# Performance work log

Hardware: AMD Instinct MI355X
Metric: run time of the kernel (lower is better)

## Reference

```python
import jax, jax.numpy as jnp
import numpy as np

N = 50000   # nodes
E = 300000  # directed edges
IN = 512
H = 256
OUT = 256
K = 4096    # K_target; since K < N, pooled node count Kc == K statically


def setup_inputs() -> dict:
    key = jax.random.key(0)
    ks = jax.random.split(key, 8)
    x = jax.random.normal(ks[0], (N, IN), jnp.float32)
    edge_index = jax.random.randint(ks[1], (2, E), 0, N)
    W1 = jax.random.normal(ks[2], (IN, H), jnp.float32) / np.float32(np.sqrt(IN))
    b1 = jnp.zeros((H,), jnp.float32)
    W2 = jax.random.normal(ks[3], (H, OUT), jnp.float32) / np.float32(np.sqrt(H))
    b2 = jnp.zeros((OUT,), jnp.float32)
    w_score = jax.random.normal(ks[4], (H,), jnp.float32) / np.float32(np.sqrt(H))
    W_skip = jax.random.normal(ks[5], (H, OUT), jnp.float32) / np.float32(np.sqrt(H))
    b_skip = jnp.zeros((OUT,), jnp.float32)
    return dict(x=x, edge_index=edge_index, W1=W1, b1=b1, W2=W2, b2=b2,
                w_score=w_score, W_skip=W_skip, b_skip=b_skip)


def _gcn_sparse(x, src, dst, W, b, n):
    # PyG GCNConv(add_self_loops=True, normalize=True): out = D^{-1/2}(A+I)D^{-1/2} x W + b,
    # degrees computed on dst after adding self loops.
    h = x @ W
    loop = jnp.arange(n)
    s = jnp.concatenate([src, loop])
    d = jnp.concatenate([dst, loop])
    deg = jax.ops.segment_sum(jnp.ones_like(d, h.dtype), d, num_segments=n)
    dinv = jnp.where(deg > 0, jax.lax.rsqrt(deg), 0.0)
    coef = (dinv[s] * dinv[d])[:, None]
    return jax.ops.segment_sum(h[s] * coef, d, num_segments=n) + b


def _forward(x, edge_index, W1, b1, W2, b2, w_score, W_skip, b_skip):
    n = x.shape[0]
    src, dst = edge_index[0], edge_index[1]

    # conv1 + relu (dropout is identity in eval mode)
    x1 = jax.nn.relu(_gcn_sparse(x, src, dst, W1, b1, n))
    raw = x1 @ w_score                       # [N] score (Linear, no bias)
    x1g = x1 * jnp.tanh(raw)[:, None]        # gated features

    # top-K node selection
    _, kept = jax.lax.top_k(raw, K)          # sorted descending, like torch.topk
    keep_mask = jnp.zeros((n,), bool).at[kept].set(True)
    deg = jax.ops.segment_sum(jnp.ones((src.shape[0],), jnp.int32), src, num_segments=n)

    # cluster ids: kept nodes get 0..K-1 in topk order
    cid = jnp.full((n,), -1, jnp.int32).at[kept].set(jnp.arange(K, dtype=jnp.int32))

    # non-kept nodes join the kept (undirected) neighbor with max degree;
    # encode (degree, -node_id) so segment_max picks max degree, tie-break smallest id
    s_all = jnp.concatenate([src, dst])
    t_all = jnp.concatenate([dst, src])
    cand = jnp.where(keep_mask[t_all], deg[t_all] * n + (n - 1 - t_all), -1)
    best = jax.ops.segment_max(cand, s_all, num_segments=n)  # empty segs -> int min
    has = best >= 0
    best_t = (n - 1) - jnp.where(has, best % n, 0)
    # global fallback: kept node with max degree (tie-break: earliest in topk order)
    enc_k = deg[kept] * K + (K - 1 - jnp.arange(K))
    bg = kept[jnp.argmax(enc_k)]
    cid = jnp.where(keep_mask, cid, jnp.where(has, cid[best_t], cid[bg]))

    # mean pooling per cluster (pool_by_partition)
    sums = jax.ops.segment_sum(x1g, cid, num_segments=K)
    cnt = jnp.maximum(jax.ops.segment_sum(jnp.ones((n,), x.dtype), cid, num_segments=K), 1.0)
    xp = sums / cnt[:, None]

    # pooled edges with dedup + self-pair removal, as dense KxK adjacency (rows = dst)
    cu, cv = cid[src], cid[dst]
    A = jnp.zeros((K, K), x.dtype).at[cv, cu].max((cu != cv).astype(x.dtype))
    Ahat = A + jnp.eye(K, dtype=x.dtype)
    di = jax.lax.rsqrt(Ahat.sum(axis=1))     # deg >= 1 from self loops
    An = di[:, None] * Ahat * di[None, :]

    # conv2 on pooled graph, broadcast back, skip connection
    xp2 = An @ (xp @ W2) + b2
    return xp2[cid] + x1 @ W_skip + b_skip


def reference(x, edge_index, W1, b1, W2, b2, w_score, W_skip, b_skip):
    return _forward(x, edge_index, W1, b1, W2, b2, w_score, W_skip, b_skip)
```

## Files before the change

### kernel.cpp

```cpp
#include <hip/hip_runtime.h>
#include <hip/hip_bf16.h>

#define N_NODES 50000
#define E_EDGES 300000
#define IN_F 512
#define H_F 256
#define OUT_F 256
#define K_CL 4096
#define KW (K_CL / 32)
#define PCH 128
#define THRESH 192
#define MAXH 1024
#define NSPL 32
#define NB2 ((N_NODES + 255) / 256)

typedef short bh8 __attribute__((ext_vector_type(8)));
typedef float f4 __attribute__((ext_vector_type(4)));
typedef unsigned short u16;

__device__ __forceinline__ unsigned fkey(float f) {
    unsigned u = __float_as_uint(f);
    return (u & 0x80000000u) ? ~u : (u | 0x80000000u);
}

__device__ __forceinline__ u16 f2bf(float f) {
    __hip_bfloat16 b = __float2bfloat16(f);
    return *reinterpret_cast<u16*>(&b);
}

__global__ __launch_bounds__(256) void init_nodes(int* cntD, int* degS,
                                                  unsigned long long* best_enc,
                                                  int* bgnode, int* heavycnt,
                                                  unsigned long long* bestpack) {
    int i = blockIdx.x * blockDim.x + threadIdx.x;
    if (i < N_NODES) { cntD[i] = 0; degS[i] = 0; best_enc[i] = 0ULL; }
    if (i == 0) { *heavycnt = 0; *bgnode = 0x7FFFFFFF; *bestpack = 0ULL; }
}

__global__ __launch_bounds__(256) void deg_edges(const int* __restrict__ src,
                                                 const int* __restrict__ dst,
                                                 int* cntD, int* degS) {
    int e = blockIdx.x * blockDim.x + threadIdx.x;
    if (e >= E_EDGES) return;
    atomicAdd(&cntD[dst[e]], 1);
    atomicAdd(&degS[src[e]], 1);
}

__global__ __launch_bounds__(256) void make_dinv(const int* __restrict__ cntD, float* dinv) {
    int i = blockIdx.x * blockDim.x + threadIdx.x;
    if (i < N_NODES) dinv[i] = rsqrtf((float)cntD[i] + 1.0f);
}

#define SBM 64
#define SBN 128
#define SBK 16
#define SAPAD 4
__global__ __launch_bounds__(256) void gemm_f32s(const float* __restrict__ A,
                                                 const float* __restrict__ B,
                                                 float* __restrict__ C,
                                                 int M, int Nc, int Kd) {
    __shared__ float As[2][SBK][SBM + SAPAD];
    __shared__ float Bs[2][SBK][SBN];
    int tid = threadIdx.x;
    int tx = tid & 15;
    int ty = tid >> 4;
    int lane = tid & 63;
    int wave = tid >> 6;
    int row0 = blockIdx.y * SBM, col0 = blockIdx.x * SBN;
    float acc[4][8] = {};

    int ar = tid >> 2;
    int akq = tid & 3;

    auto stage_B = [&](int k0, int bb) {
        #pragma unroll
        for (int u = 0; u < 2; ++u) {
            int chunk = wave * 2 + u;
            int krow = chunk * 2 + (lane >> 5);
            const float* gsrc = &B[(long)(k0 + krow) * Nc + col0 + (lane & 31) * 4];
            __builtin_amdgcn_global_load_lds(
                (const __attribute__((address_space(1))) void*)gsrc,
                (__attribute__((address_space(3))) void*)&Bs[bb][chunk * 2][0],
                16, 0, 0);
        }
    };
    auto stage_A = [&](int k0, int bb) {
        int gr = row0 + ar;
        float4 v = {0.f, 0.f, 0.f, 0.f};
        if (gr < M) v = *(const float4*)&A[(long)gr * Kd + k0 + akq * 4];
        As[bb][akq * 4 + 0][ar] = v.x;
        As[bb][akq * 4 + 1][ar] = v.y;
        As[bb][akq * 4 + 2][ar] = v.z;
        As[bb][akq * 4 + 3][ar] = v.w;
    };
    auto compute = [&](int bb) {
        #pragma unroll
        for (int k = 0; k < SBK; ++k) {
            float4 a0 = *(const float4*)&As[bb][k][ty * 4];
            float4 b0 = *(const float4*)&Bs[bb][k][tx * 4];
            float4 b1 = *(const float4*)&Bs[bb][k][tx * 4 + 64];
            float av[4] = {a0.x, a0.y, a0.z, a0.w};
            float bv[8] = {b0.x, b0.y, b0.z, b0.w, b1.x, b1.y, b1.z, b1.w};
            #pragma unroll
            for (int i = 0; i < 4; ++i)
                #pragma unroll
                for (int j = 0; j < 8; ++j)
                    acc[i][j] += av[i] * bv[j];
        }
    };

    stage_B(0, 0);
    stage_A(0, 0);
    __syncthreads();
    int nt = Kd / SBK;
    for (int t = 0; t < nt; ++t) {
        int cb = t & 1;
        if (t + 1 < nt) {
            stage_B(SBK * (t + 1), cb ^ 1);
            stage_A(SBK * (t + 1), cb ^ 1);
        }
        compute(cb);
        __syncthreads();
    }

    #pragma unroll
    for (int i = 0; i < 4; ++i) {
        int gr = row0 + ty * 4 + i;
        if (gr >= M) continue;
        float4 o0 = {acc[i][0], acc[i][1], acc[i][2], acc[i][3]};
        float4 o1 = {acc[i][4], acc[i][5], acc[i][6], acc[i][7]};
        *(float4*)&C[(long)gr * Nc + col0 + tx * 4] = o0;
        *(float4*)&C[(long)gr * Nc + col0 + 64 + tx * 4] = o1;
    }
}

__global__ __launch_bounds__(256) void conv_bf16(const float* __restrict__ src,
                                                 u16* __restrict__ dst,
                                                 const int* __restrict__ cnt, long total4) {
    long i = (long)blockIdx.x * 256 + threadIdx.x;
    if (i >= total4) return;
    float s = 1.f;
    if (cnt) { int row = (int)(i >> 6); s = 1.f / fmaxf((float)cnt[row], 1.f); }
    float4 v = ((const float4*)src)[i];
    ushort4 o;
    o.x = f2bf(v.x * s); o.y = f2bf(v.y * s);
    o.z = f2bf(v.z * s); o.w = f2bf(v.w * s);
    ((ushort4*)dst)[i] = o;
}

__global__ __launch_bounds__(256) void pack_W(const float* __restrict__ W, u16* __restrict__ Bp) {
    int k = blockIdx.x;
    int col = threadIdx.x;
    int kb = k >> 5, g = (k >> 3) & 3, j = k & 7;
    Bp[(((long)(kb * 4 + g) * 256) + col) * 8 + j] = f2bf(W[(long)k * 256 + col]);
}

__global__ __launch_bounds__(256) void gemm_mfma(const u16* __restrict__ Ab,
                                                 const u16* __restrict__ Bp,
                                                 float* __restrict__ C,
                                                 int M,
                                                 const int* __restrict__ cid,
                                                 const float* __restrict__ xp2,
                                                 const float* __restrict__ bskip) {
    int tid = threadIdx.x;
    int w = tid >> 6, l = tid & 63;
    int lo16 = l & 15, hi4 = l >> 4;
    int arow = blockIdx.x * 64 + w * 16 + lo16;
    f4 acc[16];
    #pragma unroll
    for (int n = 0; n < 16; ++n) acc[n] = (f4){0.f, 0.f, 0.f, 0.f};

    #pragma unroll
    for (int kb = 0; kb < 8; ++kb) {
        bh8 a = {0, 0, 0, 0, 0, 0, 0, 0};
        if (arow < M) a = *(const bh8*)&Ab[(long)arow * 256 + kb * 32 + hi4 * 8];
        const u16* bbase = &Bp[(((long)(kb * 4 + hi4)) * 256 + lo16) * 8];
        #pragma unroll
        for (int n = 0; n < 16; ++n) {
            bh8 b = *(const bh8*)&bbase[(long)n * 128];
            acc[n] = __builtin_amdgcn_mfma_f32_16x16x32_bf16(a, b, acc[n], 0, 0, 0);
        }
    }

    int orow0 = blockIdx.x * 64 + w * 16 + hi4 * 4;
    #pragma unroll
    for (int r = 0; r < 4; ++r) {
        int gr = orow0 + r;
        if (gr >= M) continue;
        long rb = (long)gr * 256;
        const float* xrow = cid ? (xp2 + (long)cid[gr] * 256) : nullptr;
        #pragma unroll
        for (int n = 0; n < 16; ++n) {
            int gc = n * 16 + lo16;
            float v = acc[n][r];
            if (cid) v += xrow[gc] + bskip[gc];
            C[rb + gc] = v;
        }
    }
}

__global__ __launch_bounds__(256) void scan_l1(const int* __restrict__ cnt,
                                               int* bsum, int n) {
    __shared__ int s[256];
    int t = threadIdx.x;
    int i = blockIdx.x * 256 + t;
    s[t] = (i < n) ? cnt[i] : 0;
    __syncthreads();
    for (int off = 128; off > 0; off >>= 1) {
        if (t < off) s[t] += s[t + off];
        __syncthreads();
    }
    if (t == 0) bsum[blockIdx.x] = s[0];
}

__global__ __launch_bounds__(256) void scan_l2(const int* __restrict__ bsum,
                                               int* bstart, int nb) {
    __shared__ int s[256];
    int t = threadIdx.x;
    int v = (t < nb) ? bsum[t] : 0;
    s[t] = v;
    __syncthreads();
    for (int off = 1; off < 256; off <<= 1) {
        int a = (t >= off) ? s[t - off] : 0;
        __syncthreads();
        s[t] += a;
        __syncthreads();
    }
    if (t < nb) bstart[t] = s[t] - v;
}

__global__ __launch_bounds__(256) void scan_l3(const int* __restrict__ cnt,
                                               const int* __restrict__ bstart,
                                               int* start, int* cur, int n) {
    __shared__ int s[256];
    int t = threadIdx.x;
    int i = blockIdx.x * 256 + t;
    int v = (i < n) ? cnt[i] : 0;
    s[t] = v;
    __syncthreads();
    for (int off = 1; off < 256; off <<= 1) {
        int a = (t >= off) ? s[t - off] : 0;
        __syncthreads();
        s[t] += a;
        __syncthreads();
    }
    int st = bstart[blockIdx.x] + s[t] - v;
    if (i < n) { start[i] = st; cur[i] = st; }
    if (i == n - 1) start[n] = st + v;
}

__global__ __launch_bounds__(256) void csr_scatter(const int* __restrict__ src,
                                                   const int* __restrict__ dst,
                                                   int* cur, int* csr) {
    int e = blockIdx.x * blockDim.x + threadIdx.x;
    if (e >= E_EDGES) return;
    int d = dst[e];
    int p = atomicAdd(&cur[d], 1);
    csr[p] = src[e];
}

__global__ __launch_bounds__(256) void agg_fused(const float* __restrict__ h,
                                                 const float* __restrict__ dinv,
                                                 const int* __restrict__ rowptr,
                                                 const int* __restrict__ csr,
                                                 const float* __restrict__ b1,
                                                 const float* __restrict__ w_score,
                                                 float* x1, u16* x1b, float* raw) {
    __shared__ int s_src[128];
    __shared__ float s_cf[128];
    __shared__ float red[256];
    int i = blockIdx.x, j = threadIdx.x;
    float di_ = dinv[i];
    float acc = di_ * di_ * h[(long)i * H_F + j];
    int p0 = rowptr[i], p1 = rowptr[i + 1];
    for (int base = p0; base < p1; base += 128) {
        int m = p1 - base; if (m > 128) m = 128;
        if (j < m) { int s = csr[base + j]; s_src[j] = s; s_cf[j] = dinv[s]; }
        __syncthreads();
        #pragma unroll 4
        for (int t = 0; t < m; ++t)
            acc += (s_cf[t] * di_) * h[(long)s_src[t] * H_F + j];
        __syncthreads();
    }
    float v = fmaxf(acc + b1[j], 0.f);
    x1[(long)i * H_F + j] = v;
    x1b[(long)i * H_F + j] = f2bf(v);
    red[j] = v * w_score[j];
    __syncthreads();
    for (int off = 128; off > 0; off >>= 1) {
        if (j < off) red[j] += red[j + off];
        __syncthreads();
    }
    if (j == 0) raw[i] = red[0];
}

__global__ __launch_bounds__(1024) void topk_select(const float* __restrict__ raw,
                                                    unsigned* outT, int* outNeedEq) {
    __shared__ unsigned hist[256];
    __shared__ unsigned sh_prefix;
    __shared__ int sh_k;
    int tid = threadIdx.x;
    if (tid == 0) { sh_prefix = 0; sh_k = K_CL; }
    __syncthreads();
    for (int byte = 3; byte >= 0; --byte) {
        if (tid < 256) hist[tid] = 0;
        __syncthreads();
        unsigned prefix = sh_prefix;
        unsigned known_mask = (byte == 3) ? 0u : (0xFFFFFFFFu << ((byte + 1) * 8));
        for (int i = tid; i < N_NODES; i += 1024) {
            unsigned key = fkey(raw[i]);
            if ((key & known_mask) == prefix)
                atomicAdd(&hist[(key >> (byte * 8)) & 255], 1u);
        }
        __syncthreads();
        if (tid == 0) {
            int kk = sh_k;
            int cum = 0;
            int v = 255;
            for (; v > 0; --v) {
                int c = (int)hist[v];
                if (cum + c >= kk) break;
                cum += c;
            }
            sh_prefix = prefix | ((unsigned)v << (byte * 8));
            sh_k = kk - cum;
        }
        __syncthreads();
    }
    if (tid == 0) { *outT = sh_prefix; *outNeedEq = sh_k; }
}

__global__ __launch_bounds__(256) void topk_count(const float* __restrict__ raw,
                                                  const unsigned* pT,
                                                  int* bGt, int* bEq) {
    __shared__ int sg[256], se[256];
    unsigned T = *pT;
    int t = threadIdx.x;
    int i = blockIdx.x * 256 + t;
    int gt = 0, eq = 0;
    if (i < N_NODES) {
        unsigned k = fkey(raw[i]);
        gt = k > T; eq = (k == T);
    }
    sg[t] = gt; se[t] = eq;
    __syncthreads();
    for (int off = 128; off > 0; off >>= 1) {
        if (t < off) { sg[t] += sg[t + off]; se[t] += se[t + off]; }
        __syncthreads();
    }
    if (t == 0) { bGt[blockIdx.x] = sg[0]; bEq[blockIdx.x] = se[0]; }
}

__global__ __launch_bounds__(256) void scan_blocks(const int* __restrict__ bGt,
                                                   const int* __restrict__ bEq,
                                                   int* gtStart, int* eqStart) {
    __shared__ int sg[256], se[256];
    int t = threadIdx.x;
    int vg = (t < NB2) ? bGt[t] : 0;
    int ve = (t < NB2) ? bEq[t] : 0;
    sg[t] = vg; se[t] = ve;
    __syncthreads();
    for (int off = 1; off < 256; off <<= 1) {
        int a = (t >= off) ? sg[t - off] : 0;
        int b = (t >= off) ? se[t - off] : 0;
        __syncthreads();
        sg[t] += a; se[t] += b;
        __syncthreads();
    }
    if (t < NB2) { gtStart[t] = sg[t] - vg; eqStart[t] = se[t] - ve; }
    if (t == 255) gtStart[NB2] = sg[255];
}

__global__ __launch_bounds__(256) void topk_assign(const float* __restrict__ raw,
                                                   const unsigned* pT, const int* pNeedEq,
                                                   const int* __restrict__ degS,
                                                   const int* __restrict__ gtStart,
                                                   const int* __restrict__ eqStart,
                                                   int* keep, int* cid,
                                                   unsigned long long* bestpack) {
    __shared__ int sg[256], se[256];
    unsigned T = *pT;
    int needEq = *pNeedEq;
    int totalGt = gtStart[NB2];
    int b = blockIdx.x, t = threadIdx.x;
    int i = b * 256 + t;
    int gt = 0, eq = 0;
    unsigned k = 0;
    if (i < N_NODES) {
        k = fkey(raw[i]);
        gt = k > T; eq = (k == T);
    }
    sg[t] = gt; se[t] = eq;
    __syncthreads();
    for (int off = 1; off < 256; off <<= 1) {
        int a = (t >= off) ? sg[t - off] : 0;
        int c = (t >= off) ? se[t - off] : 0;
        __syncthreads();
        sg[t] += a; se[t] += c;
        __syncthreads();
    }
    int eg = sg[t] - gt, ee = se[t] - eq;
    int kp = 0;
    unsigned long long p = 0ULL;
    if (i < N_NODES) {
        int c = -1;
        if (gt) { kp = 1; c = gtStart[b] + eg; }
        else if (eq) {
            int r = eqStart[b] + ee;
            if (r < needEq) { kp = 1; c = totalGt + r; }
        }
        keep[i] = kp; cid[i] = c;
        if (kp) p = ((unsigned long long)(unsigned)degS[i] << 32) | k;
    }
    #pragma unroll
    for (int o = 32; o > 0; o >>= 1) {
        unsigned long long q = __shfl_xor((long long)p, o, 64);
        if (q > p) p = q;
    }
    if ((t & 63) == 0 && p) atomicMax(bestpack, p);
}

__global__ __launch_bounds__(256) void bg_node(const int* __restrict__ keep,
                                               const int* __restrict__ degS,
                                               const float* __restrict__ raw,
                                               const unsigned long long* bestpack, int* bgnode) {
    int i = blockIdx.x * blockDim.x + threadIdx.x;
    if (i < N_NODES && keep[i]) {
        unsigned long long p = ((unsigned long long)(unsigned)degS[i] << 32) | fkey(raw[i]);
        if (p == *bestpack) atomicMin(bgnode, i);
    }
}

__global__ __launch_bounds__(256) void neigh_edges(const int* __restrict__ src,
                                                   const int* __restrict__ dst,
                                                   const int* __restrict__ keep,
                                                   const int* __restrict__ degS,
                                                   unsigned long long* best_enc) {
    int e = blockIdx.x * blockDim.x + threadIdx.x;
    if (e >= 2 * E_EDGES) return;
    int s, t;
    if (e < E_EDGES) { s = src[e]; t = dst[e]; }
    else { s = dst[e - E_EDGES]; t = src[e - E_EDGES]; }
    if (!keep[s] && keep[t]) {
        unsigned long long enc =
            (unsigned long long)((long long)degS[t] * N_NODES + (N_NODES - 1 - t)) + 1ULL;
        atomicMax(&best_enc[s], enc);
    }
}

__global__ __launch_bounds__(256) void resolve_cid(const int* __restrict__ keep,
                                                   const unsigned long long* __restrict__ best_enc,
                                                   const int* __restrict__ bgnode, int* cid) {
    int i = blockIdx.x * blockDim.x + threadIdx.x;
    if (i >= N_NODES) return;
    if (keep[i]) return;
    unsigned long long v = best_enc[i];
    if (v > 0ULL) {
        long long enc = (long long)(v - 1ULL);
        int t = (N_NODES - 1) - (int)(enc % N_NODES);
        cid[i] = cid[t];
    } else {
        cid[i] = cid[*bgnode];
    }
}

#define NPB 1024
__global__ __launch_bounds__(256) void ccount2(const int* __restrict__ cid, int* ccnt) {
    __shared__ int hist[K_CL];
    for (int t = threadIdx.x; t < K_CL; t += 256) hist[t] = 0;
    __syncthreads();
    int base = blockIdx.x * NPB;
    #pragma unroll
    for (int u = 0; u < NPB / 256; ++u) {
        int idx = base + u * 256 + threadIdx.x;
        if (idx < N_NODES) atomicAdd(&hist[cid[idx]], 1);
    }
    __syncthreads();
    for (int t = threadIdx.x; t < K_CL; t += 256) {
        int hh = hist[t];
        if (hh) atomicAdd(&ccnt[t], hh);
    }
}

__global__ __launch_bounds__(256) void cscatter2(const int* __restrict__ cid,
                                                 int* ccur, int* clist) {
    __shared__ int hist[K_CL];
    for (int t = threadIdx.x; t < K_CL; t += 256) hist[t] = 0;
    __syncthreads();
    int base = blockIdx.x * NPB;
    int myc[NPB / 256], myr[NPB / 256];
    #pragma unroll
    for (int u = 0; u < NPB / 256; ++u) {
        int idx = base + u * 256 + threadIdx.x;
        if (idx < N_NODES) { myc[u] = cid[idx]; myr[u] = atomicAdd(&hist[myc[u]], 1); }
        else myc[u] = -1;
    }
    __syncthreads();
    for (int t = threadIdx.x; t < K_CL; t += 256) {
        int hh = hist[t];
        if (hh) hist[t] = atomicAdd(&ccur[t], hh);
    }
    __syncthreads();
    #pragma unroll
    for (int u = 0; u < NPB / 256; ++u)
        if (myc[u] >= 0) clist[hist[myc[u]] + myr[u]] = base + u * 256 + threadIdx.x;
}

__global__ __launch_bounds__(256) void pool_chunk(const float* __restrict__ x1,
                                                  const float* __restrict__ raw,
                                                  const int* __restrict__ clist,
                                                  const int* __restrict__ cid,
                                                  float* xp) {
    __shared__ int s_node[PCH];
    __shared__ int s_c[PCH];
    __shared__ float s_g[PCH];
    int j = threadIdx.x;
    int base = blockIdx.x * PCH;
    int m = N_NODES - base; if (m > PCH) m = PCH;
    for (int t = j; t < m; t += 256) {
        int nd = clist[base + t];
        s_node[t] = nd;
        s_c[t] = cid[nd];
        s_g[t] = tanhf(raw[nd]);
    }
    __syncthreads();
    float acc = 0.f;
    int cprev = s_c[0];
    for (int t = 0; t < m; t += 4) {
        int mm = m - t; if (mm > 4) mm = 4;
        float v[4];
        #pragma unroll
        for (int u = 0; u < 4; ++u)
            if (u < mm) v[u] = x1[(long)s_node[t + u] * H_F + j];
        #pragma unroll
        for (int u = 0; u < 4; ++u) {
            if (u < mm) {
                int c = s_c[t + u];
                if (c != cprev) {
                    atomicAdd(&xp[(long)cprev * H_F + j], acc);
                    acc = 0.f;
                    cprev = c;
                }
                acc += s_g[t + u] * v[u];
            }
        }
    }
    atomicAdd(&xp[(long)cprev * H_F + j], acc);
}

__global__ __launch_bounds__(256) void build_Abits(const int* __restrict__ src,
                                                   const int* __restrict__ dst,
                                                   const int* __restrict__ cid,
                                                   unsigned* Abits) {
    int e = blockIdx.x * blockDim.x + threadIdx.x;
    if (e >= E_EDGES) return;
    int cu = cid[src[e]], cv = cid[dst[e]];
    if (cu != cv) atomicOr(&Abits[(long)cv * KW + (cu >> 5)], 1u << (cu & 31));
}

__global__ __launch_bounds__(256) void pop_di2(const unsigned* __restrict__ Abits, float* di,
                                               int* nnzA, int* heavy, int* heavycnt) {
    int i = blockIdx.x * blockDim.x + threadIdx.x;
    if (i >= K_CL) return;
    int c = 0;
    for (int w = 0; w < KW; ++w) c += __popc(Abits[(long)i * KW + w]);
    di[i] = rsqrtf((float)c + 1.0f);
    nnzA[i] = c;
    if (c > THRESH) {
        int p = atomicAdd(heavycnt, 1);
        if (p < MAXH) heavy[p] = i;
    }
}

__global__ __launch_bounds__(256) void spmm_light(const unsigned* __restrict__ Abits,
                                                  const float* __restrict__ xpW2,
                                                  const float* __restrict__ di,
                                                  const float* __restrict__ b2,
                                                  const int* __restrict__ nnzA,
                                                  float* xp2) {
    __shared__ unsigned s_row[KW];
    __shared__ float s_part[3][256];
    int cv = blockIdx.x;
    if (nnzA[cv] > THRESH) return;
    int tid = threadIdx.x;
    int w = tid >> 6, l = tid & 63;
    if (tid < KW) s_row[tid] = Abits[(long)cv * KW + tid];
    __syncthreads();
    float4 a0 = {0.f, 0.f, 0.f, 0.f}, a1 = {0.f, 0.f, 0.f, 0.f};
    const float4* Y4 = (const float4*)xpW2;
    for (int wi = w * 32; wi < w * 32 + 32; wi += 2) {
        unsigned w0 = s_row[wi], w1 = s_row[wi + 1];
        while (w0 | w1) {
            if (w0) {
                int b = __ffs(w0) - 1; w0 &= w0 - 1;
                int cu = wi * 32 + b;
                float d = di[cu];
                float4 y = Y4[(long)cu * 64 + l];
                a0.x += d * y.x; a0.y += d * y.y; a0.z += d * y.z; a0.w += d * y.w;
            }
            if (w1) {
                int b = __ffs(w1) - 1; w1 &= w1 - 1;
                int cu = (wi + 1) * 32 + b;
                float d = di[cu];
                float4 y = Y4[(long)cu * 64 + l];
                a1.x += d * y.x; a1.y += d * y.y; a1.z += d * y.z; a1.w += d * y.w;
            }
        }
    }
    float4 acc = {a0.x + a1.x, a0.y + a1.y, a0.z + a1.z, a0.w + a1.w};
    if (w > 0) *(float4*)&s_part[w - 1][l * 4] = acc;
    __syncthreads();
    if (w == 0) {
        #pragma unroll
        for (int ww = 0; ww < 3; ++ww) {
            float4 p = *(float4*)&s_part[ww][l * 4];
            acc.x += p.x; acc.y += p.y; acc.z += p.z; acc.w += p.w;
        }
        float dv = di[cv];
        float4 ys = Y4[(long)cv * 64 + l];
        float4 o;
        o.x = dv * (acc.x + dv * ys.x) + b2[l * 4 + 0];
        o.y = dv * (acc.y + dv * ys.y) + b2[l * 4 + 1];
        o.z = dv * (acc.z + dv * ys.z) + b2[l * 4 + 2];
        o.w = dv * (acc.w + dv * ys.w) + b2[l * 4 + 3];
        *(float4*)&xp2[(long)cv * H_F + l * 4] = o;
    }
}

__global__ __launch_bounds__(256) void spmm_heavy(const unsigned* __restrict__ Abits,
                                                  const float* __restrict__ xpW2,
                                                  const float* __restrict__ di,
                                                  const int* __restrict__ heavy,
                                                  const int* __restrict__ heavycnt,
                                                  float* Zacc) {
    __shared__ float s_part[3][256];
    int hi = blockIdx.x;
    int cnt = *heavycnt; if (cnt > MAXH) cnt = MAXH;
    if (hi >= cnt) return;
    int cv = heavy[hi];
    int sp = blockIdx.y;
    int tid = threadIdx.x;
    int w = tid >> 6, l = tid & 63;
    int wi = sp * (KW / NSPL) + w;
    unsigned word = Abits[(long)cv * KW + wi];
    float4 acc = {0.f, 0.f, 0.f, 0.f};
    const float4* Y4 = (const float4*)xpW2;
    while (word) {
        int b = __ffs(word) - 1; word &= word - 1;
        int cu = wi * 32 + b;
        float d = di[cu];
        float4 y = Y4[(long)cu * 64 + l];
        acc.x += d * y.x; acc.y += d * y.y; acc.z += d * y.z; acc.w += d * y.w;
    }
    if (w > 0) *(float4*)&s_part[w - 1][l * 4] = acc;
    __syncthreads();
    if (w == 0) {
        #pragma unroll
        for (int ww = 0; ww < 3; ++ww) {
            float4 p = *(float4*)&s_part[ww][l * 4];
            acc.x += p.x; acc.y += p.y; acc.z += p.z; acc.w += p.w;
        }
        float* zp = &Zacc[(long)cv * H_F + l * 4];
        atomicAdd(zp + 0, acc.x);
        atomicAdd(zp + 1, acc.y);
        atomicAdd(zp + 2, acc.z);
        atomicAdd(zp + 3, acc.w);
    }
}

__global__ __launch_bounds__(256) void heavy_epi(const float* __restrict__ Zacc,
                                                 const float* __restrict__ xpW2,
                                                 const float* __restrict__ di,
                                                 const float* __restrict__ b2,
                                                 const int* __restrict__ heavy,
                                                 const int* __restrict__ heavycnt,
                                                 float* xp2) {
    int hi = blockIdx.x;
    int cnt = *heavycnt; if (cnt > MAXH) cnt = MAXH;
    if (hi >= cnt) return;
    int cv = heavy[hi];
    int j = threadIdx.x;
    float dv = di[cv];
    xp2[(long)cv * H_F + j] =
        dv * (Zacc[(long)cv * H_F + j] + dv * xpW2[(long)cv * H_F + j]) + b2[j];
}

static inline size_t align256(size_t x) { return (x + 255) & ~(size_t)255; }

extern "C" void kernel_launch(void* const* d_in, const int* in_sizes, int n_in,
                              void* d_out, int out_size, void* d_ws, size_t ws_size,
                              hipStream_t stream) {
    const float* x      = (const float*)d_in[0];
    const int*   eidx   = (const int*)d_in[1];
    const float* W1     = (const float*)d_in[2];
    const float* b1     = (const float*)d_in[3];
    const float* W2     = (const float*)d_in[4];
    const float* b2     = (const float*)d_in[5];
    const float* wscore = (const float*)d_in[6];
    const float* Wskip  = (const float*)d_in[7];
    const float* bskip  = (const float*)d_in[8];
    float* out = (float*)d_out;

    const int* src = eidx;
    const int* dst = eidx + E_EDGES;

    char* ws = (char*)d_ws;
    size_t off = 0;
    auto alloc = [&](size_t bytes) { char* p = ws + off; off += align256(bytes); return p; };

    float* h     = (float*)alloc((size_t)N_NODES * H_F * 4);
    float* x1    = (float*)alloc((size_t)N_NODES * H_F * 4);
    u16*   x1b   = (u16*)alloc((size_t)N_NODES * H_F * 2);
    float* raw   = (float*)alloc((size_t)N_NODES * 4);
    float* dinv  = (float*)alloc((size_t)N_NODES * 4);
    int*   cntD  = (int*)alloc((size_t)N_NODES * 4);
    int*   degS  = (int*)alloc((size_t)N_NODES * 4);
    int*   keep  = (int*)alloc((size_t)N_NODES * 4);
    int*   cid   = (int*)alloc((size_t)N_NODES * 4);
    unsigned long long* best_enc = (unsigned long long*)alloc((size_t)N_NODES * 8);
    int*   rowptr= (int*)alloc((size_t)(N_NODES + 1) * 4);
    int*   cur   = (int*)alloc((size_t)N_NODES * 4);
    int*   csr   = (int*)alloc((size_t)E_EDGES * 4);
    int*   ccnt  = (int*)alloc((size_t)K_CL * 4);
    int*   cstart= (int*)alloc((size_t)(K_CL + 1) * 4);
    int*   ccur  = (int*)alloc((size_t)K_CL * 4);
    int*   clist = (int*)alloc((size_t)N_NODES * 4);
    int*   bGt   = (int*)alloc((size_t)NB2 * 4);
    int*   bEq   = (int*)alloc((size_t)NB2 * 4);
    int*   gtStart = (int*)alloc((size_t)(NB2 + 1) * 4);
    int*   eqStart = (int*)alloc((size_t)NB2 * 4);
    int*   bsum  = (int*)alloc((size_t)256 * 4);
    int*   bstart= (int*)alloc((size_t)256 * 4);
    char*  small = alloc(64);
    unsigned* selT = (unsigned*)(small + 0);
    int* needEq    = (int*)(small + 4);
    int* bgnode    = (int*)(small + 8);
    int* heavycnt  = (int*)(small + 12);
    unsigned long long* bestpack = (unsigned long long*)(small + 16);
    float* xp    = (float*)alloc((size_t)K_CL * H_F * 4);
    unsigned* Abits = (unsigned*)alloc((size_t)K_CL * KW * 4);
    float* di    = (float*)alloc((size_t)K_CL * 4);
    int*   nnzA  = (int*)alloc((size_t)K_CL * 4);
    int*   heavy = (int*)alloc((size_t)MAXH * 4);
    float* Zacc  = (float*)alloc((size_t)K_CL * H_F * 4);
    float* xpW2  = (float*)alloc((size_t)K_CL * H_F * 4);
    float* xp2   = (float*)alloc((size_t)K_CL * H_F * 4);
    u16*  xpb   = (u16*)alloc((size_t)K_CL * H_F * 2);
    u16*  BpS   = (u16*)alloc((size_t)H_F * OUT_F * 2);
    u16*  Bp2   = (u16*)alloc((size_t)H_F * H_F * 2);
    (void)ws_size; (void)n_in; (void)in_sizes; (void)out_size;

    int nb = NB2;
    int eb = (E_EDGES + 255) / 256;

    init_nodes<<<nb, 256, 0, stream>>>(cntD, degS, best_enc, bgnode, heavycnt, bestpack);
    deg_edges<<<eb, 256, 0, stream>>>(src, dst, cntD, degS);
    make_dinv<<<nb, 256, 0, stream>>>(cntD, dinv);

    pack_W<<<256, 256, 0, stream>>>(Wskip, BpS);
    pack_W<<<256, 256, 0, stream>>>(W2, Bp2);

    {
        dim3 grid(H_F / SBN, (N_NODES + SBM - 1) / SBM);
        gemm_f32s<<<grid, 256, 0, stream>>>(x, W1, h, N_NODES, H_F, IN_F);
    }

    scan_l1<<<NB2, 256, 0, stream>>>(cntD, bsum, N_NODES);
    scan_l2<<<1, 256, 0, stream>>>(bsum, bstart, NB2);
    scan_l3<<<NB2, 256, 0, stream>>>(cntD, bstart, rowptr, cur, N_NODES);
    csr_scatter<<<eb, 256, 0, stream>>>(src, dst, cur, csr);
    agg_fused<<<N_NODES, 256, 0, stream>>>(h, dinv, rowptr, csr, b1, wscore, x1, x1b, raw);

    topk_select<<<1, 1024, 0, stream>>>(raw, selT, needEq);
    topk_count<<<NB2, 256, 0, stream>>>(raw, selT, bGt, bEq);
    scan_blocks<<<1, 256, 0, stream>>>(bGt, bEq, gtStart, eqStart);
    topk_assign<<<NB2, 256, 0, stream>>>(raw, selT, needEq, degS, gtStart, eqStart,
                                         keep, cid, bestpack);
    bg_node<<<nb, 256, 0, stream>>>(keep, degS, raw, bestpack, bgnode);

    neigh_edges<<<(2 * E_EDGES + 255) / 256, 256, 0, stream>>>(src, dst, keep, degS, best_enc);
    resolve_cid<<<nb, 256, 0, stream>>>(keep, best_enc, bgnode, cid);

    hipMemsetAsync(ccnt, 0, (size_t)K_CL * 4, stream);
    {
        int cb = (N_NODES + NPB - 1) / NPB;
        ccount2<<<cb, 256, 0, stream>>>(cid, ccnt);
        scan_l1<<<K_CL / 256, 256, 0, stream>>>(ccnt, bsum, K_CL);
        scan_l2<<<1, 256, 0, stream>>>(bsum, bstart, K_CL / 256);
        scan_l3<<<K_CL / 256, 256, 0, stream>>>(ccnt, bstart, cstart, ccur, K_CL);
        cscatter2<<<cb, 256, 0, stream>>>(cid, ccur, clist);
    }
    hipMemsetAsync(xp, 0, (size_t)K_CL * H_F * 4, stream);
    pool_chunk<<<(N_NODES + PCH - 1) / PCH, 256, 0, stream>>>(x1, raw, clist, cid, xp);

    conv_bf16<<<(K_CL * (H_F / 4) + 255) / 256, 256, 0, stream>>>(
        xp, xpb, ccnt, (long)K_CL * (H_F / 4));

    gemm_mfma<<<K_CL / 64, 256, 0, stream>>>(xpb, Bp2, xpW2, K_CL,
                                             nullptr, nullptr, nullptr);

    hipMemsetAsync(Abits, 0, (size_t)K_CL * KW * 4, stream);
    hipMemsetAsync(Zacc, 0, (size_t)K_CL * H_F * 4, stream);
    build_Abits<<<eb, 256, 0, stream>>>(src, dst, cid, Abits);
    pop_di2<<<(K_CL + 255) / 256, 256, 0, stream>>>(Abits, di, nnzA, heavy, heavycnt);
    spmm_light<<<K_CL, 256, 0, stream>>>(Abits, xpW2, di, b2, nnzA, xp2);
    {
        dim3 hgrid(MAXH, NSPL);
        spmm_heavy<<<hgrid, 256, 0, stream>>>(Abits, xpW2, di, heavy, heavycnt, Zacc);
    }
    heavy_epi<<<MAXH, 256, 0, stream>>>(Zacc, xpW2, di, b2, heavy, heavycnt, xp2);

    gemm_mfma<<<(N_NODES + 63) / 64, 256, 0, stream>>>(x1b, BpS, out, N_NODES,
                                                       cid, xp2, bskip);
}
```

Before: 732.5 us.

## Fuse bf16 conversion into GEMM, merge weight packing, defer A-tile LDS writes

The mean-scale and bf16 conversion of pooled features moves into the MFMA GEMM's A-operand load, which removes the conv_bf16 kernel and its intermediate buffer. The two pack_W launches become one launch with a doubled grid. In the fp32 SIMT GEMM, A-tile global loads are now held in registers and written to LDS after compute, so global load latency overlaps with the FMA loop. The cost is extra registers and a runtime branch inside the MFMA kernel.

```diff
diff --git a/kernel.cpp b/kernel.cpp
--- a/kernel.cpp
+++ b/kernel.cpp
@@ -71,6 +71,7 @@
 
     int ar = tid >> 2;
     int akq = tid & 3;
+    float4 ra;
 
     auto stage_B = [&](int k0, int bb) {
         #pragma unroll
@@ -84,14 +85,17 @@
                 16, 0, 0);
         }
     };
-    auto stage_A = [&](int k0, int bb) {
+    auto stage_A_load = [&](int k0) {
         int gr = row0 + ar;
         float4 v = {0.f, 0.f, 0.f, 0.f};
         if (gr < M) v = *(const float4*)&A[(long)gr * Kd + k0 + akq * 4];
-        As[bb][akq * 4 + 0][ar] = v.x;
-        As[bb][akq * 4 + 1][ar] = v.y;
-        As[bb][akq * 4 + 2][ar] = v.z;
-        As[bb][akq * 4 + 3][ar] = v.w;
+        ra = v;
+    };
+    auto stage_A_write = [&](int bb) {
+        As[bb][akq * 4 + 0][ar] = ra.x;
+        As[bb][akq * 4 + 1][ar] = ra.y;
+        As[bb][akq * 4 + 2][ar] = ra.z;
+        As[bb][akq * 4 + 3][ar] = ra.w;
     };
     auto compute = [&](int bb) {
         #pragma unroll
@@ -110,16 +114,18 @@
     };
 
     stage_B(0, 0);
-    stage_A(0, 0);
+    stage_A_load(0);
+    stage_A_write(0);
     __syncthreads();
     int nt = Kd / SBK;
     for (int t = 0; t < nt; ++t) {
         int cb = t & 1;
         if (t + 1 < nt) {
             stage_B(SBK * (t + 1), cb ^ 1);
-            stage_A(SBK * (t + 1), cb ^ 1);
+            stage_A_load(SBK * (t + 1));
         }
         compute(cb);
+        if (t + 1 < nt) stage_A_write(cb ^ 1);
         __syncthreads();
     }
 
@@ -134,28 +140,19 @@
     }
 }
 
-__global__ __launch_bounds__(256) void conv_bf16(const float* __restrict__ src,
-                                                 u16* __restrict__ dst,
-                                                 const int* __restrict__ cnt, long total4) {
-    long i = (long)blockIdx.x * 256 + threadIdx.x;
-    if (i >= total4) return;
-    float s = 1.f;
-    if (cnt) { int row = (int)(i >> 6); s = 1.f / fmaxf((float)cnt[row], 1.f); }
-    float4 v = ((const float4*)src)[i];
-    ushort4 o;
-    o.x = f2bf(v.x * s); o.y = f2bf(v.y * s);
-    o.z = f2bf(v.z * s); o.w = f2bf(v.w * s);
-    ((ushort4*)dst)[i] = o;
-}
-
-__global__ __launch_bounds__(256) void pack_W(const float* __restrict__ W, u16* __restrict__ Bp) {
-    int k = blockIdx.x;
+__global__ __launch_bounds__(256) void pack_W2(const float* __restrict__ Wa, u16* Bpa,
+                                               const float* __restrict__ Wb, u16* Bpb) {
+    int k = blockIdx.x & 255;
+    const float* W = (blockIdx.x < 256) ? Wa : Wb;
+    u16* Bp = (blockIdx.x < 256) ? Bpa : Bpb;
     int col = threadIdx.x;
     int kb = k >> 5, g = (k >> 3) & 3, j = k & 7;
     Bp[(((long)(kb * 4 + g) * 256) + col) * 8 + j] = f2bf(W[(long)k * 256 + col]);
 }
 
 __global__ __launch_bounds__(256) void gemm_mfma(const u16* __restrict__ Ab,
+                                                 const float* __restrict__ Af32,
+                                                 const int* __restrict__ cnt,
                                                  const u16* __restrict__ Bp,
                                                  float* __restrict__ C,
                                                  int M,
@@ -170,10 +167,23 @@
     #pragma unroll
     for (int n = 0; n < 16; ++n) acc[n] = (f4){0.f, 0.f, 0.f, 0.f};
 
+    float s = 1.f;
+    if (Af32 && arow < M) s = 1.f / fmaxf((float)cnt[arow], 1.f);
+
     #pragma unroll
     for (int kb = 0; kb < 8; ++kb) {
         bh8 a = {0, 0, 0, 0, 0, 0, 0, 0};
-        if (arow < M) a = *(const bh8*)&Ab[(long)arow * 256 + kb * 32 + hi4 * 8];
+        if (arow < M) {
+            if (Af32) {
+                float4 v0 = *(const float4*)&Af32[(long)arow * 256 + kb * 32 + hi4 * 8];
+                float4 v1 = *(const float4*)&Af32[(long)arow * 256 + kb * 32 + hi4 * 8 + 4];
+                u16 tmp[8] = {f2bf(v0.x * s), f2bf(v0.y * s), f2bf(v0.z * s), f2bf(v0.w * s),
+                              f2bf(v1.x * s), f2bf(v1.y * s), f2bf(v1.z * s), f2bf(v1.w * s)};
+                a = *(const bh8*)tmp;
+            } else {
+                a = *(const bh8*)&Ab[(long)arow * 256 + kb * 32 + hi4 * 8];
+            }
+        }
         const u16* bbase = &Bp[(((long)(kb * 4 + hi4)) * 256 + lo16) * 8];
         #pragma unroll
         for (int n = 0; n < 16; ++n) {
@@ -745,7 +755,6 @@
     float* Zacc  = (float*)alloc((size_t)K_CL * H_F * 4);
     float* xpW2  = (float*)alloc((size_t)K_CL * H_F * 4);
     float* xp2   = (float*)alloc((size_t)K_CL * H_F * 4);
-    u16*  xpb   = (u16*)alloc((size_t)K_CL * H_F * 2);
     u16*  BpS   = (u16*)alloc((size_t)H_F * OUT_F * 2);
     u16*  Bp2   = (u16*)alloc((size_t)H_F * H_F * 2);
     (void)ws_size; (void)n_in; (void)in_sizes; (void)out_size;
@@ -757,8 +766,7 @@
     deg_edges<<<eb, 256, 0, stream>>>(src, dst, cntD, degS);
     make_dinv<<<nb, 256, 0, stream>>>(cntD, dinv);
 
-    pack_W<<<256, 256, 0, stream>>>(Wskip, BpS);
-    pack_W<<<256, 256, 0, stream>>>(W2, Bp2);
+    pack_W2<<<512, 256, 0, stream>>>(Wskip, BpS, W2, Bp2);
 
     {
         dim3 grid(H_F / SBN, (N_NODES + SBM - 1) / SBM);
@@ -793,10 +801,7 @@
     hipMemsetAsync(xp, 0, (size_t)K_CL * H_F * 4, stream);
     pool_chunk<<<(N_NODES + PCH - 1) / PCH, 256, 0, stream>>>(x1, raw, clist, cid, xp);
 
-    conv_bf16<<<(K_CL * (H_F / 4) + 255) / 256, 256, 0, stream>>>(
-        xp, xpb, ccnt, (long)K_CL * (H_F / 4));
-
-    gemm_mfma<<<K_CL / 64, 256, 0, stream>>>(xpb, Bp2, xpW2, K_CL,
+    gemm_mfma<<<K_CL / 64, 256, 0, stream>>>(nullptr, xp, ccnt, Bp2, xpW2, K_CL,
                                              nullptr, nullptr, nullptr);
 
     hipMemsetAsync(Abits, 0, (size_t)K_CL * KW * 4, stream);
@@ -810,6 +815,6 @@
     }
     heavy_epi<<<MAXH, 256, 0, stream>>>(Zacc, xpW2, di, b2, heavy, heavycnt, xp2);
 
-    gemm_mfma<<<(N_NODES + 63) / 64, 256, 0, stream>>>(x1b, BpS, out, N_NODES,
-                                                       cid, xp2, bskip);
-}
+    gemm_mfma<<<(N_NODES + 63) / 64, 256, 0, stream>>>(x1b, nullptr, nullptr, BpS, out,
+                                                       N_NODES, cid, xp2, bskip);
+}
```

Result: no change. 744.2 us (+1.6%).
